# Kernel tuning notes

Measured on AMD Instinct MI355X. Metric: run time of the kernel, lower is better.

The kernel has to match this reference:

```python
import jax, jax.numpy as jnp
import numpy as np


def setup_inputs() -> dict:
    key = jax.random.key(0)
    ks = jax.random.split(key, 8)
    B, T, U = 4, 400, 80
    De, Dd, V = 512, 512, 1024
    F = De + Dd  # in_features = 1024
    s = lambda k, shape: jax.random.normal(k, shape, dtype=jnp.float32) * 0.05
    return {
        "encoder_output": jax.random.normal(ks[0], (B, T, De), dtype=jnp.float32),
        "decoder_output": jax.random.normal(ks[1], (B, U, Dd), dtype=jnp.float32),
        "W_enc": s(ks[2], (F, De)),
        "b_enc": s(ks[3], (F,)),
        "W_dec": s(ks[4], (F, Dd)),
        "b_dec": s(ks[5], (F,)),
        "W_fc": s(ks[6], (V, F)),
        "b_fc": s(ks[7], (V,)),
    }


def reference(encoder_output, decoder_output, W_enc, b_enc, W_dec, b_dec, W_fc, b_fc):
    # fc_enc / fc_dec projections: (B,T,F) and (B,U,F)
    enc = jnp.einsum("btd,fd->btf", encoder_output, W_enc) + b_enc
    dec = jnp.einsum("bud,fd->buf", decoder_output, W_dec) + b_dec
    # broadcast-add -> (B,T,U,F)
    combined = enc[:, :, None, :] + dec[:, None, :, :]
    # fc: tanh then linear -> (B,T,U,V)
    vocab_logits = jnp.einsum("btuf,vf->btuv", jnp.tanh(combined), W_fc) + b_fc
    # HAT branch: blank prob via sigmoid of logit 0
    blk_logit = vocab_logits[..., :1]
    log_blk = jax.nn.log_sigmoid(blk_logit)          # log(sigmoid)
    log_not_blk = jax.nn.log_sigmoid(-blk_logit)     # log(1 - sigmoid)
    vocab_log_probs = log_not_blk + jax.nn.log_softmax(vocab_logits[..., 1:], axis=-1)
    return jnp.concatenate([log_blk, vocab_log_probs], axis=-1)
```

## Files before the change

### kernel.cpp

```cpp
#include <hip/hip_runtime.h>
#include <hip/hip_bf16.h>
#include <cstdint>
#include <cstddef>

typedef short bf16x8 __attribute__((ext_vector_type(8)));
typedef float f32x4 __attribute__((ext_vector_type(4)));

static __device__ __forceinline__ unsigned short f2bf(float f) {
    union { float f; uint32_t u; } c; c.f = f;
    uint32_t r = c.u + 0x7FFFu + ((c.u >> 16) & 1u);
    return (unsigned short)(r >> 16);
}

static __device__ __forceinline__ float fast_tanh(float x) {
    float e = __expf(2.0f * x);
    return 1.0f - 2.0f / (e + 1.0f);
}

static __device__ __forceinline__ float softplus_f(float x) {
    return fmaxf(x, 0.0f) + log1pf(__expf(-fabsf(x)));
}

static __device__ __forceinline__ unsigned swz(unsigned a) {
    return a ^ (((a >> 7) & 7u) << 4);
}

#define GLOAD_LDS16(g, l) \
    __builtin_amdgcn_global_load_lds((const __attribute__((address_space(1))) void*)(g), \
                                     (__attribute__((address_space(3))) void*)(l), 16, 0, 0)

__global__ __launch_bounds__(256) void k_convert(
    const float* __restrict__ s0, const float* __restrict__ s1,
    const float* __restrict__ s2, const float* __restrict__ s3,
    const float* __restrict__ s4,
    unsigned short* __restrict__ d0, unsigned short* __restrict__ d1,
    unsigned short* __restrict__ d2, unsigned short* __restrict__ d3,
    unsigned short* __restrict__ d4,
    int n0, int n1, int n2, int n3, int n4)
{
    int i = blockIdx.x * 256 + threadIdx.x;
    int c0 = n0 >> 2, c1 = c0 + (n1 >> 2), c2 = c1 + (n2 >> 2),
        c3 = c2 + (n3 >> 2), c4 = c3 + (n4 >> 2);
    if (i >= c4) return;
    const float* s; unsigned short* d; int j;
    if (i < c0)      { s = s0; d = d0; j = i; }
    else if (i < c1) { s = s1; d = d1; j = i - c0; }
    else if (i < c2) { s = s2; d = d2; j = i - c1; }
    else if (i < c3) { s = s3; d = d3; j = i - c2; }
    else             { s = s4; d = d4; j = i - c3; }
    float4 v = reinterpret_cast<const float4*>(s)[j];
    ushort4 o;
    o.x = f2bf(v.x); o.y = f2bf(v.y); o.z = f2bf(v.z); o.w = f2bf(v.w);
    reinterpret_cast<ushort4*>(d)[j] = o;
}

__global__ __launch_bounds__(256) void k_proj(
    const unsigned short* __restrict__ A,
    const unsigned short* __restrict__ W,
    const float* __restrict__ bias,
    float* __restrict__ out)
{
    __shared__ unsigned short As[32 * 512];
    const int tid = threadIdx.x;
    const int m0 = blockIdx.x * 32;
    const int c0 = blockIdx.y * 128;
    {
        int row = tid >> 3;
        const unsigned short* src = A + (size_t)(m0 + row) * 512;
        unsigned int base = row * 1024;
        unsigned int sw = (row & 7) << 4;
        #pragma unroll
        for (int c = 0; c < 8; ++c) {
            int col = (tid & 7) * 8 + c * 64;
            bf16x8 v = *reinterpret_cast<const bf16x8*>(src + col);
            *reinterpret_cast<bf16x8*>(
                reinterpret_cast<char*>(As) + ((base + col * 2) ^ sw)) = v;
        }
    }
    __syncthreads();
    const int w = tid >> 6, l = tid & 63;
    const int lr = l & 15, lkb = (l >> 4) * 8;
    f32x4 acc[2][2] = {};
    const int colbase = c0 + w * 32;
    const unsigned short* Wb = W + (size_t)(colbase + lr) * 512 + lkb;
    const unsigned int sw = (lr & 7) << 4;
    for (int ks = 0; ks < 16; ++ks) {
        unsigned int kb = (ks * 32 + lkb) * 2;
        bf16x8 a0 = *reinterpret_cast<const bf16x8*>(
            reinterpret_cast<const char*>(As) + ((lr * 1024 + kb) ^ sw));
        bf16x8 a1 = *reinterpret_cast<const bf16x8*>(
            reinterpret_cast<const char*>(As) + (((16 + lr) * 1024 + kb) ^ sw));
        #pragma unroll
        for (int nf = 0; nf < 2; ++nf) {
            bf16x8 b = *reinterpret_cast<const bf16x8*>(Wb + nf * 16 * 512 + ks * 32);
            acc[0][nf] = __builtin_amdgcn_mfma_f32_16x16x32_bf16(a0, b, acc[0][nf], 0, 0, 0);
            acc[1][nf] = __builtin_amdgcn_mfma_f32_16x16x32_bf16(a1, b, acc[1][nf], 0, 0, 0);
        }
    }
    const int qr = (l >> 4) * 4;
    #pragma unroll
    for (int nf = 0; nf < 2; ++nf) {
        int col = colbase + nf * 16 + lr;
        float bv = bias[col];
        #pragma unroll
        for (int mf = 0; mf < 2; ++mf)
            #pragma unroll
            for (int r = 0; r < 4; ++r)
                out[(size_t)(m0 + mf * 16 + qr + r) * 1024 + col] = acc[mf][nf][r] + bv;
    }
}

__global__ __launch_bounds__(512, 2) void k_main(
    const float* __restrict__ enc,
    const float* __restrict__ dec,
    const unsigned short* __restrict__ Wfc,
    const float* __restrict__ bfc,
    float* __restrict__ out)
{
    extern __shared__ char smem[];
    char* Bs0 = smem;
    char* Bs1 = smem + 65536;
    char* As0 = smem + 131072;
    char* As1 = smem + 135168;
    float* red  = (float*)(smem + 139264);
    float* l0sh = (float*)(smem + 141312);

    const int tid = threadIdx.x;
    const int w = tid >> 6, l = tid & 63;
    const int lr = l & 15, q = l >> 4;
    const int r0 = blockIdx.x * 64;

    const int arow = tid >> 3;
    const float4* epv;
    const float4* dpv;
    {
        int m = r0 + arow;
        int bt = m / 80;
        int u  = m - bt * 80;
        int b  = bt / 400;
        epv = (const float4*)(enc + (size_t)bt * 1024 + (tid & 7) * 4);
        dpv = (const float4*)(dec + (size_t)(b * 80 + u) * 1024 + (tid & 7) * 4);
    }
    const unsigned awoff = swz((unsigned)(arow * 64 + (tid & 7) * 8));

    const unsigned loff  = ((unsigned)l * 16u) ^ ((((unsigned)l >> 3) & 7u) << 4);
    const unsigned vbase = (unsigned)w * 128u + (loff >> 6);
    const unsigned kbe   = (loff & 63u) >> 1;
    const unsigned short* gB = Wfc + (size_t)vbase * 1024 + kbe;

    unsigned aoff[4], boff[8];
    #pragma unroll
    for (int mf = 0; mf < 4; ++mf)
        aoff[mf] = swz((unsigned)(((mf * 16 + lr) << 6) | (q << 4)));
    #pragma unroll
    for (int nf = 0; nf < 8; ++nf)
        boff[nf] = swz((unsigned)(((w * 128 + nf * 16 + lr) << 6) | (q << 4)));

    f32x4 acc[4][8] = {};

    {
        #pragma unroll
        for (int i = 0; i < 8; ++i)
            GLOAD_LDS16(gB + i * 16 * 1024, Bs0 + w * 8192 + i * 1024);
        float4 e0 = epv[0], d0 = dpv[0];
        union { unsigned short h[4]; uint2 u; } pk;
        pk.h[0] = f2bf(fast_tanh(e0.x + d0.x));
        pk.h[1] = f2bf(fast_tanh(e0.y + d0.y));
        pk.h[2] = f2bf(fast_tanh(e0.z + d0.z));
        pk.h[3] = f2bf(fast_tanh(e0.w + d0.w));
        *(uint2*)(As0 + awoff) = pk.u;
    }
    __syncthreads();

    char* Bcur = Bs0; char* Bnxt = Bs1;
    char* Acur = As0; char* Anxt = As1;

    for (int ks = 0; ks < 32; ++ks) {
        const bool pre = (ks < 31);
        float4 e0, d0;
        if (pre) {
            e0 = epv[(ks + 1) * 8];
            d0 = dpv[(ks + 1) * 8];
            const unsigned short* g = gB + (ks + 1) * 32;
            #pragma unroll
            for (int i = 0; i < 8; ++i)
                GLOAD_LDS16(g + i * 16 * 1024, Bnxt + w * 8192 + i * 1024);
        }
        bf16x8 a[4];
        #pragma unroll
        for (int mf = 0; mf < 4; ++mf)
            a[mf] = *(const bf16x8*)(Acur + aoff[mf]);
        #pragma unroll
        for (int nf = 0; nf < 8; ++nf) {
            bf16x8 b = *(const bf16x8*)(Bcur + boff[nf]);
            #pragma unroll
            for (int mf = 0; mf < 4; ++mf)
                acc[mf][nf] = __builtin_amdgcn_mfma_f32_16x16x32_bf16(a[mf], b, acc[mf][nf], 0, 0, 0);
        }
        if (pre) {
            union { unsigned short h[4]; uint2 u; } pk;
            pk.h[0] = f2bf(fast_tanh(e0.x + d0.x));
            pk.h[1] = f2bf(fast_tanh(e0.y + d0.y));
            pk.h[2] = f2bf(fast_tanh(e0.z + d0.z));
            pk.h[3] = f2bf(fast_tanh(e0.w + d0.w));
            *(uint2*)(Anxt + awoff) = pk.u;
        }
        __syncthreads();
        char* t;
        t = Bcur; Bcur = Bnxt; Bnxt = t;
        t = Acur; Acur = Anxt; Anxt = t;
    }

    #pragma unroll
    for (int nf = 0; nf < 8; ++nf) {
        float bv = bfc[w * 128 + nf * 16 + lr];
        #pragma unroll
        for (int mf = 0; mf < 4; ++mf)
            #pragma unroll
            for (int r = 0; r < 4; ++r)
                acc[mf][nf][r] += bv;
    }
    const bool excl = (w == 0 && lr == 0);
    if (excl) {
        #pragma unroll
        for (int mf = 0; mf < 4; ++mf)
            #pragma unroll
            for (int r = 0; r < 4; ++r)
                l0sh[mf * 16 + q * 4 + r] = acc[mf][0][r];
    }
    float Mrow[4][4];
    #pragma unroll
    for (int mf = 0; mf < 4; ++mf)
        #pragma unroll
        for (int r = 0; r < 4; ++r) {
            float m = -3.0e38f;
            #pragma unroll
            for (int nf = 0; nf < 8; ++nf)
                if (!(excl && nf == 0)) m = fmaxf(m, acc[mf][nf][r]);
            #pragma unroll
            for (int s = 1; s < 16; s <<= 1)
                m = fmaxf(m, __shfl_xor(m, s, 16));
            if (lr == 0) red[(mf * 16 + q * 4 + r) * 8 + w] = m;
        }
    __syncthreads();
    #pragma unroll
    for (int mf = 0; mf < 4; ++mf)
        #pragma unroll
        for (int r = 0; r < 4; ++r) {
            int row = mf * 16 + q * 4 + r;
            float m = red[row * 8 + 0];
            #pragma unroll
            for (int j = 1; j < 8; ++j) m = fmaxf(m, red[row * 8 + j]);
            Mrow[mf][r] = m;
        }
    __syncthreads();
    #pragma unroll
    for (int mf = 0; mf < 4; ++mf)
        #pragma unroll
        for (int r = 0; r < 4; ++r) {
            float s = 0.0f;
            #pragma unroll
            for (int nf = 0; nf < 8; ++nf)
                if (!(excl && nf == 0)) s += __expf(acc[mf][nf][r] - Mrow[mf][r]);
            #pragma unroll
            for (int sh = 1; sh < 16; sh <<= 1)
                s += __shfl_xor(s, sh, 16);
            if (lr == 0) red[(mf * 16 + q * 4 + r) * 8 + w] = s;
        }
    __syncthreads();
    #pragma unroll
    for (int mf = 0; mf < 4; ++mf)
        #pragma unroll
        for (int r = 0; r < 4; ++r) {
            int row = mf * 16 + q * 4 + r;
            float s = red[row * 8 + 0];
            #pragma unroll
            for (int j = 1; j < 8; ++j) s += red[row * 8 + j];
            float lse = Mrow[mf][r] + __logf(s);
            float l0 = l0sh[row];
            float lnb = -softplus_f(l0);
            float* op = out + (size_t)(r0 + row) * 1024;
            #pragma unroll
            for (int nf = 0; nf < 8; ++nf) {
                int col = w * 128 + nf * 16 + lr;
                float val = (col == 0) ? (-softplus_f(-l0))
                                       : (acc[mf][nf][r] - lse + lnb);
                op[col] = val;
            }
        }
}

extern "C" void kernel_launch(void* const* d_in, const int* in_sizes, int n_in,
                              void* d_out, int out_size, void* d_ws, size_t ws_size,
                              hipStream_t stream)
{
    const float* encoder = (const float*)d_in[0];
    const float* decoder = (const float*)d_in[1];
    const float* W_enc   = (const float*)d_in[2];
    const float* b_enc   = (const float*)d_in[3];
    const float* W_dec   = (const float*)d_in[4];
    const float* b_dec   = (const float*)d_in[5];
    const float* W_fc    = (const float*)d_in[6];
    const float* b_fc    = (const float*)d_in[7];
    float* out = (float*)d_out;

    char* ws = (char*)d_ws;
    float*          enc_f  = (float*)(ws);
    float*          dec_f  = (float*)(ws + 6553600);
    unsigned short* Wfc_h  = (unsigned short*)(ws + 7864320);
    unsigned short* Wenc_h = (unsigned short*)(ws + 9961472);
    unsigned short* Wdec_h = (unsigned short*)(ws + 11010048);
    unsigned short* encI_h = (unsigned short*)(ws + 12058624);
    unsigned short* decI_h = (unsigned short*)(ws + 13697024);

    const int nEnc = 4 * 400 * 512, nDec = 4 * 80 * 512;
    const int nWe = 1024 * 512, nWd = 1024 * 512, nWf = 1024 * 1024;
    const int totalF4 = (nEnc + nDec + nWe + nWd + nWf) >> 2;
    k_convert<<<(totalF4 + 255) / 256, 256, 0, stream>>>(
        encoder, decoder, W_enc, W_dec, W_fc,
        encI_h, decI_h, Wenc_h, Wdec_h, Wfc_h,
        nEnc, nDec, nWe, nWd, nWf);

    k_proj<<<dim3(1600 / 32, 8), 256, 0, stream>>>(encI_h, Wenc_h, b_enc, enc_f);
    k_proj<<<dim3(320 / 32, 8), 256, 0, stream>>>(decI_h, Wdec_h, b_dec, dec_f);

    const int SMEM_BYTES = 141568;
    hipFuncSetAttribute(reinterpret_cast<const void*>(k_main),
                        hipFuncAttributeMaxDynamicSharedMemorySize, SMEM_BYTES);
    k_main<<<2000, 512, SMEM_BYTES, stream>>>(enc_f, dec_f, Wfc_h, b_fc, out);
}
```

Measured before the change: 675.6 us.

## Stage full tanh A tile in LDS once and stream W_fc directly to registers

The main kernel now computes the whole 64x1024 tanh(enc+dec) tile up front into LDS (128KB, XOR-swizzled), then runs the K loop with no barriers. The W_fc operand is no longer staged through LDS with global_load_lds; each wave loads its B fragments straight from global into registers, double-buffered across even and odd k-steps. This removes the per-step __syncthreads and the LDS round trip for weights. In exchange, each B fragment load is strided by row and depends on L2 hits, register pressure rises from holding two sets of B fragments, and the A-tile prologue is serialized before any MFMA work.

```diff
diff --git a/kernel.cpp b/kernel.cpp
--- a/kernel.cpp
+++ b/kernel.cpp
@@ -20,14 +20,6 @@
 static __device__ __forceinline__ float softplus_f(float x) {
     return fmaxf(x, 0.0f) + log1pf(__expf(-fabsf(x)));
 }
-
-static __device__ __forceinline__ unsigned swz(unsigned a) {
-    return a ^ (((a >> 7) & 7u) << 4);
-}
-
-#define GLOAD_LDS16(g, l) \
-    __builtin_amdgcn_global_load_lds((const __attribute__((address_space(1))) void*)(g), \
-                                     (__attribute__((address_space(3))) void*)(l), 16, 0, 0)
 
 __global__ __launch_bounds__(256) void k_convert(
     const float* __restrict__ s0, const float* __restrict__ s1,
@@ -118,97 +110,93 @@
     float* __restrict__ out)
 {
     extern __shared__ char smem[];
-    char* Bs0 = smem;
-    char* Bs1 = smem + 65536;
-    char* As0 = smem + 131072;
-    char* As1 = smem + 135168;
-    float* red  = (float*)(smem + 139264);
-    float* l0sh = (float*)(smem + 141312);
+    char* As   = smem;
+    float* red  = (float*)(smem + 131072);
+    float* l0sh = (float*)(smem + 133120);
 
     const int tid = threadIdx.x;
     const int w = tid >> 6, l = tid & 63;
     const int lr = l & 15, q = l >> 4;
     const int r0 = blockIdx.x * 64;
 
-    const int arow = tid >> 3;
-    const float4* epv;
-    const float4* dpv;
     {
-        int m = r0 + arow;
+        int row = tid >> 3, kc = tid & 7;
+        int m = r0 + row;
         int bt = m / 80;
         int u  = m - bt * 80;
         int b  = bt / 400;
-        epv = (const float4*)(enc + (size_t)bt * 1024 + (tid & 7) * 4);
-        dpv = (const float4*)(dec + (size_t)(b * 80 + u) * 1024 + (tid & 7) * 4);
-    }
-    const unsigned awoff = swz((unsigned)(arow * 64 + (tid & 7) * 8));
-
-    const unsigned loff  = ((unsigned)l * 16u) ^ ((((unsigned)l >> 3) & 7u) << 4);
-    const unsigned vbase = (unsigned)w * 128u + (loff >> 6);
-    const unsigned kbe   = (loff & 63u) >> 1;
-    const unsigned short* gB = Wfc + (size_t)vbase * 1024 + kbe;
-
-    unsigned aoff[4], boff[8];
-    #pragma unroll
-    for (int mf = 0; mf < 4; ++mf)
-        aoff[mf] = swz((unsigned)(((mf * 16 + lr) << 6) | (q << 4)));
+        const float* ep = enc + (size_t)bt * 1024 + kc * 8;
+        const float* dp = dec + (size_t)(b * 80 + u) * 1024 + kc * 8;
+        unsigned base = row * 2048 + kc * 16;
+        unsigned sw = (row & 7) << 4;
+        #pragma unroll
+        for (int c = 0; c < 16; ++c) {
+            float4 e0 = *(const float4*)(ep + c * 64);
+            float4 e1 = *(const float4*)(ep + c * 64 + 4);
+            float4 f0 = *(const float4*)(dp + c * 64);
+            float4 f1 = *(const float4*)(dp + c * 64 + 4);
+            union { unsigned short h[8]; bf16x8 v; } pk;
+            pk.h[0] = f2bf(fast_tanh(e0.x + f0.x));
+            pk.h[1] = f2bf(fast_tanh(e0.y + f0.y));
+            pk.h[2] = f2bf(fast_tanh(e0.z + f0.z));
+            pk.h[3] = f2bf(fast_tanh(e0.w + f0.w));
+            pk.h[4] = f2bf(fast_tanh(e1.x + f1.x));
+            pk.h[5] = f2bf(fast_tanh(e1.y + f1.y));
+            pk.h[6] = f2bf(fast_tanh(e1.z + f1.z));
+            pk.h[7] = f2bf(fast_tanh(e1.w + f1.w));
+            *(bf16x8*)(As + ((base + c * 128) ^ sw)) = pk.v;
+        }
+    }
+    __syncthreads();
+
+    const unsigned short* Wb = Wfc + (size_t)(w * 128 + lr) * 1024 + q * 8;
+    const unsigned sw = (lr & 7) << 4;
+
+    f32x4 acc[4][8] = {};
+    bf16x8 B0[8], B1[8];
+
     #pragma unroll
     for (int nf = 0; nf < 8; ++nf)
-        boff[nf] = swz((unsigned)(((w * 128 + nf * 16 + lr) << 6) | (q << 4)));
-
-    f32x4 acc[4][8] = {};
-
-    {
-        #pragma unroll
-        for (int i = 0; i < 8; ++i)
-            GLOAD_LDS16(gB + i * 16 * 1024, Bs0 + w * 8192 + i * 1024);
-        float4 e0 = epv[0], d0 = dpv[0];
-        union { unsigned short h[4]; uint2 u; } pk;
-        pk.h[0] = f2bf(fast_tanh(e0.x + d0.x));
-        pk.h[1] = f2bf(fast_tanh(e0.y + d0.y));
-        pk.h[2] = f2bf(fast_tanh(e0.z + d0.z));
-        pk.h[3] = f2bf(fast_tanh(e0.w + d0.w));
-        *(uint2*)(As0 + awoff) = pk.u;
-    }
-    __syncthreads();
-
-    char* Bcur = Bs0; char* Bnxt = Bs1;
-    char* Acur = As0; char* Anxt = As1;
-
-    for (int ks = 0; ks < 32; ++ks) {
-        const bool pre = (ks < 31);
-        float4 e0, d0;
-        if (pre) {
-            e0 = epv[(ks + 1) * 8];
-            d0 = dpv[(ks + 1) * 8];
-            const unsigned short* g = gB + (ks + 1) * 32;
-            #pragma unroll
-            for (int i = 0; i < 8; ++i)
-                GLOAD_LDS16(g + i * 16 * 1024, Bnxt + w * 8192 + i * 1024);
-        }
-        bf16x8 a[4];
-        #pragma unroll
-        for (int mf = 0; mf < 4; ++mf)
-            a[mf] = *(const bf16x8*)(Acur + aoff[mf]);
-        #pragma unroll
-        for (int nf = 0; nf < 8; ++nf) {
-            bf16x8 b = *(const bf16x8*)(Bcur + boff[nf]);
+        B0[nf] = *(const bf16x8*)(Wb + nf * 16384);
+    #pragma unroll
+    for (int nf = 0; nf < 8; ++nf)
+        B1[nf] = *(const bf16x8*)(Wb + nf * 16384 + 32);
+
+    #pragma unroll
+    for (int kp = 0; kp < 16; ++kp) {
+        const int ks0 = 2 * kp, ks1 = 2 * kp + 1;
+        {
+            bf16x8 a[4];
             #pragma unroll
             for (int mf = 0; mf < 4; ++mf)
-                acc[mf][nf] = __builtin_amdgcn_mfma_f32_16x16x32_bf16(a[mf], b, acc[mf][nf], 0, 0, 0);
-        }
-        if (pre) {
-            union { unsigned short h[4]; uint2 u; } pk;
-            pk.h[0] = f2bf(fast_tanh(e0.x + d0.x));
-            pk.h[1] = f2bf(fast_tanh(e0.y + d0.y));
-            pk.h[2] = f2bf(fast_tanh(e0.z + d0.z));
-            pk.h[3] = f2bf(fast_tanh(e0.w + d0.w));
-            *(uint2*)(Anxt + awoff) = pk.u;
-        }
-        __syncthreads();
-        char* t;
-        t = Bcur; Bcur = Bnxt; Bnxt = t;
-        t = Acur; Acur = Anxt; Anxt = t;
+                a[mf] = *(const bf16x8*)(As +
+                    (((unsigned)(lr * 2048 + mf * 32768 + q * 16 + ks0 * 64)) ^ sw));
+            #pragma unroll
+            for (int nf = 0; nf < 8; ++nf) {
+                #pragma unroll
+                for (int mf = 0; mf < 4; ++mf)
+                    acc[mf][nf] = __builtin_amdgcn_mfma_f32_16x16x32_bf16(
+                        a[mf], B0[nf], acc[mf][nf], 0, 0, 0);
+                if (ks0 + 2 < 32)
+                    B0[nf] = *(const bf16x8*)(Wb + nf * 16384 + (ks0 + 2) * 32);
+            }
+        }
+        {
+            bf16x8 a[4];
+            #pragma unroll
+            for (int mf = 0; mf < 4; ++mf)
+                a[mf] = *(const bf16x8*)(As +
+                    (((unsigned)(lr * 2048 + mf * 32768 + q * 16 + ks1 * 64)) ^ sw));
+            #pragma unroll
+            for (int nf = 0; nf < 8; ++nf) {
+                #pragma unroll
+                for (int mf = 0; mf < 4; ++mf)
+                    acc[mf][nf] = __builtin_amdgcn_mfma_f32_16x16x32_bf16(
+                        a[mf], B1[nf], acc[mf][nf], 0, 0, 0);
+                if (ks1 + 2 < 32)
+                    B1[nf] = *(const bf16x8*)(Wb + nf * 16384 + (ks1 + 2) * 32);
+            }
+        }
     }
 
     #pragma unroll
@@ -324,7 +312,7 @@
     k_proj<<<dim3(1600 / 32, 8), 256, 0, stream>>>(encI_h, Wenc_h, b_enc, enc_f);
     k_proj<<<dim3(320 / 32, 8), 256, 0, stream>>>(decI_h, Wdec_h, b_dec, dec_f);
 
-    const int SMEM_BYTES = 141568;
+    const int SMEM_BYTES = 133376;
     hipFuncSetAttribute(reinterpret_cast<const void*>(k_main),
                         hipFuncAttributeMaxDynamicSharedMemorySize, SMEM_BYTES);
     k_main<<<2000, 512, SMEM_BYTES, stream>>>(enc_f, dec_f, Wfc_h, b_fc, out);
```

Result: slower. 786.8 us (+16.5%).
